# Optimization experiments

Measured on AMD Instinct MI355X. Metric: run time of the kernel, lower is better.

The kernel has to match this reference:

```python
import jax, jax.numpy as jnp
import numpy as np

B, S, H, I, E, K = 4, 2048, 2048, 5632, 8, 2


def setup_inputs() -> dict:
    key = jax.random.key(0)
    k0, k1, k2, k3, k4 = jax.random.split(key, 5)
    std_p = 1.0 / np.sqrt(H)
    return {
        "hidden_states": jax.random.normal(k0, (B, S, H), dtype=jnp.float32),
        "router_w": jax.random.normal(k1, (E, H), dtype=jnp.float32) * 0.02,
        "w_gate": jax.random.normal(k2, (E, H, I), dtype=jnp.float32) * std_p,
        "w_up": jax.random.normal(k3, (E, H, I), dtype=jnp.float32) * std_p,
        "w_down": jax.random.normal(k4, (E, I, H), dtype=jnp.float32) * (1.0 / np.sqrt(I)),
    }


def reference(hidden_states, router_w, w_gate, w_up, w_down):
    b, s, h = hidden_states.shape
    x = hidden_states.reshape(-1, h)                       # [T, H]
    router_logits = x @ router_w.T                          # [T, E]
    routing_weights = jax.nn.softmax(router_logits, axis=-1)
    top_w, top_i = jax.lax.top_k(routing_weights, K)        # [T, K]
    top_w = top_w / jnp.sum(top_w, axis=-1, keepdims=True)  # renormalize over top-k
    # combine[t, e] = sum_k top_w[t, k] * (top_i[t, k] == e)
    combine = jnp.sum(jax.nn.one_hot(top_i, E, dtype=top_w.dtype) * top_w[..., None], axis=1)  # [T, E]
    out = jnp.zeros_like(x)
    for e in range(E):  # small fixed expert count
        # SwiGLU expert MLP: down(silu(gate(x)) * up(x))
        act = jax.nn.silu(x @ w_gate[e]) * (x @ w_up[e])    # [T, I]
        out = out + (act @ w_down[e]) * combine[:, e:e + 1]
    return (out.reshape(b, s, h),
            router_logits.reshape(b, s, E),
            top_i.reshape(b, s, K),
            top_w.reshape(b, s, K))
```

## Files before the change

### kernel.cpp

```cpp
#include <hip/hip_runtime.h>
#include <hip/hip_bf16.h>
#include <stdint.h>

#define NTOK 8192
#define HD   2048
#define ID   5632
#define NE   8
#define NASSIGN (NTOK * 2)
#define MAXT256 (NASSIGN / 256 + NE)

typedef __attribute__((ext_vector_type(8))) short  bf16x8;
typedef __attribute__((ext_vector_type(4))) float  f32x4;
typedef __attribute__((ext_vector_type(8))) unsigned short u16x8;

__device__ __forceinline__ unsigned short f2bf(float f) {
  union { float f; unsigned int u; } c; c.f = f;
  unsigned int lsb = (c.u >> 16) & 1u;
  return (unsigned short)((c.u + 0x7fffu + lsb) >> 16);
}
__device__ __forceinline__ float bf2f(unsigned short u) {
  union { float f; unsigned int u; } c; c.u = ((unsigned int)u) << 16;
  return c.f;
}

__device__ __forceinline__ void async16(const void* g, void* l) {
  __builtin_amdgcn_global_load_lds(
      (const __attribute__((address_space(1))) void*)g,
      (__attribute__((address_space(3))) void*)l, 16, 0, 0);
}

__global__ __launch_bounds__(256) void k_router(
    const float* __restrict__ x, const float* __restrict__ rw,
    float* __restrict__ out_logits, float* __restrict__ out_topi,
    float* __restrict__ out_topw,
    int* __restrict__ tk_e, float* __restrict__ tk_w, int* __restrict__ cnts)
{
  const int wid = threadIdx.x >> 6, lane = threadIdx.x & 63;
  const int t = blockIdx.x * 4 + wid;
  const float* xr = x + (size_t)t * HD;
  float acc[NE];
#pragma unroll
  for (int e = 0; e < NE; e++) acc[e] = 0.f;
#pragma unroll
  for (int i = 0; i < 8; i++) {
    const int col = lane * 4 + i * 256;
    const float4 xv = *(const float4*)(xr + col);
#pragma unroll
    for (int e = 0; e < NE; e++) {
      const float4 wv = *(const float4*)(rw + e * HD + col);
      acc[e] += xv.x * wv.x + xv.y * wv.y + xv.z * wv.z + xv.w * wv.w;
    }
  }
#pragma unroll
  for (int e = 0; e < NE; e++)
    for (int o = 32; o >= 1; o >>= 1) acc[e] += __shfl_xor(acc[e], o, 64);

  if (lane == 0) {
    int i1 = 0;
#pragma unroll
    for (int e = 1; e < NE; e++) if (acc[e] > acc[i1]) i1 = e;
    int i2 = (i1 == 0) ? 1 : 0;
#pragma unroll
    for (int e = 0; e < NE; e++) if (e != i1 && acc[e] > acc[i2]) i2 = e;
    float p2 = __expf(acc[i2] - acc[i1]);
    float s  = 1.f + p2;
    float w1 = 1.f / s, w2 = p2 / s;
#pragma unroll
    for (int e = 0; e < NE; e++) out_logits[(size_t)t * NE + e] = acc[e];
    out_topi[t * 2 + 0] = (float)i1; out_topi[t * 2 + 1] = (float)i2;
    out_topw[t * 2 + 0] = w1;        out_topw[t * 2 + 1] = w2;
    tk_e[t * 2 + 0] = i1; tk_e[t * 2 + 1] = i2;
    tk_w[t * 2 + 0] = w1; tk_w[t * 2 + 1] = w2;
    atomicAdd(&cnts[i1], 1); atomicAdd(&cnts[i2], 1);
  }
}

__global__ void k_scan(const int* __restrict__ cnts, int* __restrict__ offs,
                       int* __restrict__ cursor, int* __restrict__ tile_e,
                       int* __restrict__ tile_rt, int* __restrict__ ntiles) {
  if (threadIdx.x == 0) {
    int s = 0, nt = 0;
    for (int e = 0; e < NE; e++) {
      offs[e] = s; cursor[e] = s;
      int ntl = (cnts[e] + 255) >> 8;
      for (int i = 0; i < ntl; i++) { tile_e[nt] = e; tile_rt[nt] = i; nt++; }
      s += cnts[e];
    }
    ntiles[0] = nt;
  }
}

__global__ void k_assign(const int* __restrict__ tk_e, const float* __restrict__ tk_w,
                         int* __restrict__ cursor, int* __restrict__ perm,
                         float* __restrict__ pw, int* __restrict__ inv) {
  int t = blockIdx.x * 256 + threadIdx.x;
  if (t >= NTOK) return;
#pragma unroll
  for (int k = 0; k < 2; k++) {
    int e = tk_e[t * 2 + k];
    int pos = atomicAdd(&cursor[e], 1);
    perm[pos] = t;
    pw[pos] = tk_w[t * 2 + k];
    inv[t * 2 + k] = pos;
  }
}

__global__ __launch_bounds__(256) void k_gather(const float* __restrict__ x,
    const int* __restrict__ perm, unsigned short* __restrict__ xg) {
  const int r = blockIdx.x;
  const int tok = perm[r];
  const float* src = x + (size_t)tok * HD;
  unsigned short* dst = xg + (size_t)r * HD;
  const int c = threadIdx.x * 8;
  float4 a = *(const float4*)(src + c);
  float4 b = *(const float4*)(src + c + 4);
  u16x8 o;
  o[0] = f2bf(a.x); o[1] = f2bf(a.y); o[2] = f2bf(a.z); o[3] = f2bf(a.w);
  o[4] = f2bf(b.x); o[5] = f2bf(b.y); o[6] = f2bf(b.z); o[7] = f2bf(b.w);
  *(u16x8*)(dst + c) = o;
}

__global__ __launch_bounds__(256) void k_conv_gu(const float* __restrict__ wg,
    const float* __restrict__ wu, unsigned short* __restrict__ wgT,
    unsigned short* __restrict__ wuT) {
  __shared__ float tl[32][33];
  const int z = blockIdx.z, e = z >> 1;
  const float* in = ((z & 1) ? wu : wg) + (size_t)e * HD * ID;
  unsigned short* out = ((z & 1) ? wuT : wgT) + (size_t)e * (size_t)ID * HD;
  const int tx = threadIdx.x & 31, ty = threadIdx.x >> 5;
  const int c0 = blockIdx.x * 32, r0 = blockIdx.y * 32;
#pragma unroll
  for (int j = 0; j < 4; j++)
    tl[ty + j * 8][tx] = in[(size_t)(r0 + ty + j * 8) * ID + (c0 + tx)];
  __syncthreads();
#pragma unroll
  for (int j = 0; j < 4; j++) {
    int oc = ty + j * 8;
    out[(size_t)(c0 + oc) * HD + (r0 + tx)] = f2bf(tl[tx][oc]);
  }
}

__global__ __launch_bounds__(256) void k_conv_d(const float* __restrict__ wd,
    unsigned short* __restrict__ wdT) {
  __shared__ float tl[32][33];
  const int e = blockIdx.z;
  const float* in = wd + (size_t)e * ID * HD;
  unsigned short* out = wdT + (size_t)e * (size_t)HD * ID;
  const int tx = threadIdx.x & 31, ty = threadIdx.x >> 5;
  const int c0 = blockIdx.x * 32, r0 = blockIdx.y * 32;
#pragma unroll
  for (int j = 0; j < 4; j++)
    tl[ty + j * 8][tx] = in[(size_t)(r0 + ty + j * 8) * HD + (c0 + tx)];
  __syncthreads();
#pragma unroll
  for (int j = 0; j < 4; j++) {
    int oc = ty + j * 8;
    out[(size_t)(c0 + oc) * ID + (r0 + tx)] = f2bf(tl[tx][oc]);
  }
}

#define HB(b,kh,op) (((((b)*2+(kh))*2)+(op))*16384)

template <int EPI, int NMAT, int KMAT>
__global__ __launch_bounds__(512, 2) void k_gemm256(
    const unsigned short* __restrict__ A, const unsigned short* __restrict__ Wbase,
    const int* __restrict__ cnts, const int* __restrict__ offs,
    const int* __restrict__ tile_e, const int* __restrict__ tile_rt,
    const int* __restrict__ ntiles,
    unsigned short* __restrict__ gtmp, unsigned short* __restrict__ gact,
    const float* __restrict__ pw, float* __restrict__ dbuf)
{
  const int ti = blockIdx.y;
  if (ti >= ntiles[0]) return;
  const int e = tile_e[ti], rt = tile_rt[ti];
  const int cnt = cnts[e], off = offs[e];
  const int ct = blockIdx.x;
  const int tid = threadIdx.x;

  __shared__ __align__(16) char smem[131072];

  const unsigned short* W = Wbase + (size_t)e * (size_t)NMAT * KMAT;
  const size_t arow0 = (size_t)off + (size_t)rt * 256;
  const size_t bcol0 = (size_t)ct * 256;

  const int u0 = tid, u1 = 512 + tid;
  const int r0s = ((u0 >> 3) << 1) | (((u0 >> 2) & 1) ^ ((u0 >> 4) & 1));
  const int c0s = ((u0 & 3) ^ (r0s & 3)) * 8;
  const int r1s = ((u1 >> 3) << 1) | (((u1 >> 2) & 1) ^ ((u1 >> 4) & 1));
  const int c1s = ((u1 & 3) ^ (r1s & 3)) * 8;

  const int NT = KMAT / 64, NIT = NT / 2;

  auto STAGE_A = [&](int bb, int kh, int kt) {
    const int kc = kt * 64 + kh * 32;
    async16(A + (arow0 + r0s) * (size_t)KMAT + kc + c0s, smem + HB(bb,kh,0) + tid * 16);
    async16(A + (arow0 + r1s) * (size_t)KMAT + kc + c1s, smem + HB(bb,kh,0) + 8192 + tid * 16);
  };
  auto STAGE_B = [&](int bb, int kh, int kt) {
    const int kc = kt * 64 + kh * 32;
    async16(W + (bcol0 + r0s) * (size_t)KMAT + kc + c0s, smem + HB(bb,kh,1) + tid * 16);
    async16(W + (bcol0 + r1s) * (size_t)KMAT + kc + c1s, smem + HB(bb,kh,1) + 8192 + tid * 16);
  };

  f32x4 acc[8][4];
#pragma unroll
  for (int m = 0; m < 8; m++)
#pragma unroll
    for (int n = 0; n < 4; n++) acc[m][n] = (f32x4)0.f;

  const int lane = tid & 63, wid = tid >> 6;
  const int wm = wid >> 2, wn = wid & 3;
  const int fr = lane & 15;
  const int slotp = (lane >> 4) ^ (fr & 3);
  const int laddr = ((fr << 6) | (slotp << 4)) ^ ((fr & 4) << 4);

  STAGE_A(0,0,0); STAGE_B(0,0,0); STAGE_A(0,1,0); STAGE_B(0,1,0);
  STAGE_A(1,0,1); STAGE_B(1,0,1);
  asm volatile("s_waitcnt vmcnt(4)");
  asm volatile("s_barrier" ::: "memory");

  constexpr int SB[8]  = {1,1,0,0,0,0,1,1};
  constexpr int SOP[8] = {0,1,0,1,0,1,0,1};
  constexpr int SKH[8] = {1,1,0,0,1,1,0,0};
  constexpr int SKO[8] = {1,1,2,2,2,2,3,3};

  bf16x8 bfr[4];
  for (int i = 0; i < NIT; ++i) {
#pragma unroll
    for (int p = 0; p < 8; ++p) {
      const int b = p >> 2, kh = (p >> 1) & 1, mh = p & 1;
      bf16x8 afr[4];
#pragma unroll
      for (int t = 0; t < 4; t++)
        afr[t] = *(const bf16x8*)(smem + HB(b,kh,0) + ((wm*128 + mh*64 + t*16) << 6) + laddr);
      if (mh == 0) {
#pragma unroll
        for (int t = 0; t < 4; t++)
          bfr[t] = *(const bf16x8*)(smem + HB(b,kh,1) + ((wn*64 + t*16) << 6) + laddr);
      }
      {
        int kt = 2 * i + SKO[p]; kt = kt < NT - 1 ? kt : NT - 1;
        if (SOP[p] == 0) STAGE_A(SB[p], SKH[p], kt);
        else             STAGE_B(SB[p], SKH[p], kt);
      }
      asm volatile("s_barrier" ::: "memory");
      __builtin_amdgcn_s_setprio(1);
#pragma unroll
      for (int t = 0; t < 4; t++)
#pragma unroll
        for (int n = 0; n < 4; n++)
          acc[mh*4 + t][n] = __builtin_amdgcn_mfma_f32_16x16x32_bf16(afr[t], bfr[n], acc[mh*4 + t][n], 0, 0, 0);
      __builtin_amdgcn_s_setprio(0);
      if (p == 3 || p == 7) asm volatile("s_waitcnt vmcnt(4)");
      asm volatile("s_barrier" ::: "memory");
    }
  }
  asm volatile("s_waitcnt vmcnt(0)");

  const int crow = (lane >> 4) * 4, ccol = lane & 15;
  const int rbase = rt * 256 + wm * 128;
#pragma unroll
  for (int mt = 0; mt < 8; ++mt) {
#pragma unroll
    for (int j = 0; j < 4; ++j) {
      const int rl = rbase + mt * 16 + crow + j;
      if (rl >= cnt) continue;
      const size_t grow = (size_t)off + rl;
      float wgt = 0.f;
      if (EPI == 2) wgt = pw[grow];
#pragma unroll
      for (int nt = 0; nt < 4; ++nt) {
        const int col = (int)bcol0 + wn * 64 + nt * 16 + ccol;
        const float v = acc[mt][nt][j];
        if (EPI == 0) {
          gtmp[grow * (size_t)NMAT + col] = f2bf(v);
        } else if (EPI == 1) {
          const float g = bf2f(gtmp[grow * (size_t)NMAT + col]);
          const float a = g / (1.f + __expf(-g)) * v;
          gact[grow * (size_t)NMAT + col] = f2bf(a);
        } else {
          dbuf[grow * (size_t)NMAT + col] = v * wgt;
        }
      }
    }
  }
}

__global__ __launch_bounds__(256) void k_combine(const float* __restrict__ dbuf,
    const int* __restrict__ inv, float* __restrict__ out) {
  const int t = blockIdx.x;
  const int p0 = inv[t * 2], p1 = inv[t * 2 + 1];
  const float4* r0 = (const float4*)(dbuf + (size_t)p0 * HD);
  const float4* r1 = (const float4*)(dbuf + (size_t)p1 * HD);
  float4* o = (float4*)(out + (size_t)t * HD);
#pragma unroll
  for (int i = 0; i < 2; i++) {
    int c = threadIdx.x + i * 256;
    float4 a = r0[c], b = r1[c];
    o[c] = make_float4(a.x + b.x, a.y + b.y, a.z + b.z, a.w + b.w);
  }
}

extern "C" void kernel_launch(void* const* d_in, const int* in_sizes, int n_in,
                              void* d_out, int out_size, void* d_ws, size_t ws_size,
                              hipStream_t stream) {
  const float* x  = (const float*)d_in[0];
  const float* rw = (const float*)d_in[1];
  const float* wg = (const float*)d_in[2];
  const float* wu = (const float*)d_in[3];
  const float* wd = (const float*)d_in[4];

  float* outp       = (float*)d_out;
  float* out_logits = outp + (size_t)NTOK * HD;
  float* out_topi   = out_logits + (size_t)NTOK * NE;
  float* out_topw   = out_topi + (size_t)NTOK * 2;

  char* w = (char*)d_ws;
  int*   cnts    = (int*)(w + 0);
  int*   offs    = (int*)(w + 64);
  int*   cursor  = (int*)(w + 128);
  int*   ntiles  = (int*)(w + 192);
  int*   tile_e  = (int*)(w + 256);
  int*   tile_rt = (int*)(w + 1280);
  int*   tk_e    = (int*)(w + 4096);
  float* tk_w    = (float*)(w + 4096 + 65536);
  int*   perm    = (int*)(w + 4096 + 2 * 65536);
  float* pw      = (float*)(w + 4096 + 3 * 65536);
  int*   inv     = (int*)(w + 4096 + 4 * 65536);

  char* big = w + (1 << 20);
  unsigned short* xg = (unsigned short*)big;
  const size_t XG_E = (size_t)(NASSIGN + 256) * HD;
  unsigned short* wgT = xg + XG_E;
  const size_t WT_E = (size_t)NE * ID * HD;
  unsigned short* wuT  = wgT + WT_E;
  unsigned short* wdT  = wuT + WT_E;
  unsigned short* gtmp = wdT + WT_E;
  const size_t GA_E = (size_t)(NASSIGN + 256) * ID;
  unsigned short* gact = gtmp + GA_E;
  float* dbuf = (float*)(gact + GA_E);

  hipMemsetAsync(d_ws, 0, 256, stream);

  k_conv_gu<<<dim3(ID / 32, HD / 32, 2 * NE), 256, 0, stream>>>(wg, wu, wgT, wuT);
  k_conv_d<<<dim3(HD / 32, ID / 32, NE), 256, 0, stream>>>(wd, wdT);

  k_router<<<NTOK / 4, 256, 0, stream>>>(x, rw, out_logits, out_topi, out_topw,
                                         tk_e, tk_w, cnts);
  k_scan<<<1, 64, 0, stream>>>(cnts, offs, cursor, tile_e, tile_rt, ntiles);
  k_assign<<<NTOK / 256, 256, 0, stream>>>(tk_e, tk_w, cursor, perm, pw, inv);
  k_gather<<<NASSIGN, 256, 0, stream>>>(x, perm, xg);

  k_gemm256<0, ID, HD><<<dim3(ID / 256, MAXT256), 512, 0, stream>>>(
      xg, wgT, cnts, offs, tile_e, tile_rt, ntiles, gtmp, nullptr, nullptr, nullptr);
  k_gemm256<1, ID, HD><<<dim3(ID / 256, MAXT256), 512, 0, stream>>>(
      xg, wuT, cnts, offs, tile_e, tile_rt, ntiles, gtmp, gact, nullptr, nullptr);
  k_gemm256<2, HD, ID><<<dim3(HD / 256, MAXT256), 512, 0, stream>>>(
      gact, wdT, cnts, offs, tile_e, tile_rt, ntiles, nullptr, nullptr, pw, dbuf);

  k_combine<<<NTOK, 256, 0, stream>>>(dbuf, inv, outp);
}
```

Before: 2.030 ms.

## Fuse gate and up GEMMs into one kernel sharing A tiles

Merges the separate gate and up projection GEMMs into a single kernel. Each A tile is loaded once and multiplied against both the gate and up weights, with two accumulator sets and the SiLU*up epilogue applied in registers. This removes the bf16 gate intermediate write and read, and halves A-tile traffic for those GEMMs. The grid is also reordered so row tiles vary fastest. The cost is double the accumulator registers and occupancy limited to one block per CU, plus a new three-buffer pipeline with 32-wide k steps.

```diff
diff --git a/kernel.cpp b/kernel.cpp
--- a/kernel.cpp
+++ b/kernel.cpp
@@ -17,10 +17,6 @@
   union { float f; unsigned int u; } c; c.f = f;
   unsigned int lsb = (c.u >> 16) & 1u;
   return (unsigned short)((c.u + 0x7fffu + lsb) >> 16);
-}
-__device__ __forceinline__ float bf2f(unsigned short u) {
-  union { float f; unsigned int u; } c; c.u = ((unsigned int)u) << 16;
-  return c.f;
 }
 
 __device__ __forceinline__ void async16(const void* g, void* l) {
@@ -159,27 +155,24 @@
   }
 }
 
-#define HB(b,kh,op) (((((b)*2+(kh))*2)+(op))*16384)
-
-template <int EPI, int NMAT, int KMAT>
-__global__ __launch_bounds__(512, 2) void k_gemm256(
-    const unsigned short* __restrict__ A, const unsigned short* __restrict__ Wbase,
+__global__ __launch_bounds__(512, 1) void k_gemm_gu256(
+    const unsigned short* __restrict__ A,
+    const unsigned short* __restrict__ BgT, const unsigned short* __restrict__ BuT,
     const int* __restrict__ cnts, const int* __restrict__ offs,
     const int* __restrict__ tile_e, const int* __restrict__ tile_rt,
-    const int* __restrict__ ntiles,
-    unsigned short* __restrict__ gtmp, unsigned short* __restrict__ gact,
-    const float* __restrict__ pw, float* __restrict__ dbuf)
+    const int* __restrict__ ntiles, unsigned short* __restrict__ gact)
 {
-  const int ti = blockIdx.y;
+  const int ti = blockIdx.x;
   if (ti >= ntiles[0]) return;
   const int e = tile_e[ti], rt = tile_rt[ti];
   const int cnt = cnts[e], off = offs[e];
-  const int ct = blockIdx.x;
+  const int ct = blockIdx.y;
   const int tid = threadIdx.x;
 
-  __shared__ __align__(16) char smem[131072];
-
-  const unsigned short* W = Wbase + (size_t)e * (size_t)NMAT * KMAT;
+  __shared__ __align__(16) char smem[9 * 16384];
+
+  const unsigned short* Bg = BgT + (size_t)e * (size_t)ID * HD;
+  const unsigned short* Bu = BuT + (size_t)e * (size_t)ID * HD;
   const size_t arow0 = (size_t)off + (size_t)rt * 256;
   const size_t bcol0 = (size_t)ct * 256;
 
@@ -189,17 +182,136 @@
   const int r1s = ((u1 >> 3) << 1) | (((u1 >> 2) & 1) ^ ((u1 >> 4) & 1));
   const int c1s = ((u1 & 3) ^ (r1s & 3)) * 8;
 
-  const int NT = KMAT / 64, NIT = NT / 2;
+  auto ST = [&](const unsigned short* P, size_t row0, int kc, int chunk) {
+    async16(P + (row0 + r0s) * (size_t)HD + kc + c0s, smem + (chunk << 14) + tid * 16);
+    async16(P + (row0 + r1s) * (size_t)HD + kc + c1s, smem + (chunk << 14) + 8192 + tid * 16);
+  };
+
+  f32x4 accg[8][4], accu[8][4];
+#pragma unroll
+  for (int m = 0; m < 8; m++)
+#pragma unroll
+    for (int n = 0; n < 4; n++) { accg[m][n] = (f32x4)0.f; accu[m][n] = (f32x4)0.f; }
+
+  const int lane = tid & 63, wid = tid >> 6;
+  const int wm = wid >> 2, wn = wid & 3;
+  const int fr = lane & 15;
+  const int slotp = (lane >> 4) ^ (fr & 3);
+  const int laddr = ((fr << 6) | (slotp << 4)) ^ ((fr & 4) << 4);
+
+  const int NT = HD / 32;
+
+  ST(A, arow0, 0, 0);  ST(Bg, bcol0, 0, 1);  ST(Bu, bcol0, 0, 2);
+  ST(A, arow0, 32, 3); ST(Bg, bcol0, 32, 4); ST(Bu, bcol0, 32, 5);
+  asm volatile("s_waitcnt vmcnt(6)");
+  asm volatile("s_barrier" ::: "memory");
+
+#define MFMA16(ACC, MB, FRG) \
+  __builtin_amdgcn_s_setprio(1); \
+  _Pragma("unroll") \
+  for (int t = 0; t < 4; t++) \
+    _Pragma("unroll") \
+    for (int n = 0; n < 4; n++) \
+      ACC[(MB) + t][n] = __builtin_amdgcn_mfma_f32_16x16x32_bf16(afr[t], FRG[n], ACC[(MB) + t][n], 0, 0, 0); \
+  __builtin_amdgcn_s_setprio(0);
+
+  int cb = 0, sb = 2;
+  bf16x8 afr[4], bgr[4], bur[4];
+  for (int i = 0; i < NT; ++i) {
+    const int cb3 = cb * 3, sb3 = sb * 3;
+    int kn = i + 2; kn = kn < NT - 1 ? kn : NT - 1;
+    const int kc2 = kn * 32;
+#pragma unroll
+    for (int t = 0; t < 4; t++)
+      afr[t] = *(const bf16x8*)(smem + ((cb3 + 0) << 14) + ((wm * 128 + t * 16) << 6) + laddr);
+#pragma unroll
+    for (int t = 0; t < 4; t++)
+      bgr[t] = *(const bf16x8*)(smem + ((cb3 + 1) << 14) + ((wn * 64 + t * 16) << 6) + laddr);
+    ST(A, arow0, kc2, sb3 + 0);
+    asm volatile("s_barrier" ::: "memory");
+    MFMA16(accg, 0, bgr)
+    asm volatile("s_barrier" ::: "memory");
+#pragma unroll
+    for (int t = 0; t < 4; t++)
+      bur[t] = *(const bf16x8*)(smem + ((cb3 + 2) << 14) + ((wn * 64 + t * 16) << 6) + laddr);
+    ST(Bg, bcol0, kc2, sb3 + 1);
+    asm volatile("s_barrier" ::: "memory");
+    MFMA16(accu, 0, bur)
+    asm volatile("s_barrier" ::: "memory");
+#pragma unroll
+    for (int t = 0; t < 4; t++)
+      afr[t] = *(const bf16x8*)(smem + ((cb3 + 0) << 14) + ((wm * 128 + 64 + t * 16) << 6) + laddr);
+    ST(Bu, bcol0, kc2, sb3 + 2);
+    asm volatile("s_barrier" ::: "memory");
+    MFMA16(accg, 4, bgr)
+    asm volatile("s_barrier" ::: "memory");
+    asm volatile("s_waitcnt vmcnt(6)");
+    MFMA16(accu, 4, bur)
+    asm volatile("s_barrier" ::: "memory");
+    sb = cb; cb = cb + 1 == 3 ? 0 : cb + 1;
+  }
+  asm volatile("s_waitcnt vmcnt(0)");
+
+  const int crow = (lane >> 4) * 4, ccol = lane & 15;
+  const int rbase = rt * 256 + wm * 128;
+#pragma unroll
+  for (int mt = 0; mt < 8; ++mt) {
+#pragma unroll
+    for (int j = 0; j < 4; ++j) {
+      const int rl = rbase + mt * 16 + crow + j;
+      if (rl >= cnt) continue;
+      const size_t grow = (size_t)off + rl;
+#pragma unroll
+      for (int nt = 0; nt < 4; ++nt) {
+        const int col = (int)bcol0 + wn * 64 + nt * 16 + ccol;
+        const float g = accg[mt][nt][j], u = accu[mt][nt][j];
+        const float a = g / (1.f + __expf(-g)) * u;
+        gact[grow * (size_t)ID + col] = f2bf(a);
+      }
+    }
+  }
+#undef MFMA16
+}
+
+#define HB(b,kh,op) (((((b)*2+(kh))*2)+(op))*16384)
+__global__ __launch_bounds__(512, 2) void k_gemm_dn256(
+    const unsigned short* __restrict__ A,
+    const unsigned short* __restrict__ Wbase,
+    const int* __restrict__ cnts, const int* __restrict__ offs,
+    const int* __restrict__ tile_e, const int* __restrict__ tile_rt,
+    const int* __restrict__ ntiles,
+    const float* __restrict__ pw, float* __restrict__ dbuf)
+{
+  const int ti = blockIdx.x;
+  if (ti >= ntiles[0]) return;
+  const int e = tile_e[ti], rt = tile_rt[ti];
+  const int cnt = cnts[e], off = offs[e];
+  const int ct = blockIdx.y;
+  const int tid = threadIdx.x;
+
+  __shared__ __align__(16) char smem[131072];
+
+  const unsigned short* W = Wbase + (size_t)e * (size_t)HD * ID;
+  const size_t arow0 = (size_t)off + (size_t)rt * 256;
+  const size_t bcol0 = (size_t)ct * 256;
+
+  const int u0 = tid, u1 = 512 + tid;
+  const int r0s = ((u0 >> 3) << 1) | (((u0 >> 2) & 1) ^ ((u0 >> 4) & 1));
+  const int c0s = ((u0 & 3) ^ (r0s & 3)) * 8;
+  const int r1s = ((u1 >> 3) << 1) | (((u1 >> 2) & 1) ^ ((u1 >> 4) & 1));
+  const int c1s = ((u1 & 3) ^ (r1s & 3)) * 8;
+
+  const int NT = ID / 64, NIT = NT / 2;
 
   auto STAGE_A = [&](int bb, int kh, int kt) {
     const int kc = kt * 64 + kh * 32;
-    async16(A + (arow0 + r0s) * (size_t)KMAT + kc + c0s, smem + HB(bb,kh,0) + tid * 16);
-    async16(A + (arow0 + r1s) * (size_t)KMAT + kc + c1s, smem + HB(bb,kh,0) + 8192 + tid * 16);
+    async16(A + (arow0 + r0s) * (size_t)ID + kc + c0s, smem + HB(bb,kh,0) + tid * 16);
+    async16(A + (arow0 + r1s) * (size_t)ID + kc + c1s, smem + HB(bb,kh,0) + 8192 + tid * 16);
   };
   auto STAGE_B = [&](int bb, int kh, int kt) {
     const int kc = kt * 64 + kh * 32;
-    async16(W + (bcol0 + r0s) * (size_t)KMAT + kc + c0s, smem + HB(bb,kh,1) + tid * 16);
-    async16(W + (bcol0 + r1s) * (size_t)KMAT + kc + c1s, smem + HB(bb,kh,1) + 8192 + tid * 16);
+    async16(W + (bcol0 + r0s) * (size_t)ID + kc + c0s, smem + HB(bb,kh,1) + tid * 16);
+    async16(W + (bcol0 + r1s) * (size_t)ID + kc + c1s, smem + HB(bb,kh,1) + 8192 + tid * 16);
   };
 
   f32x4 acc[8][4];
@@ -266,21 +378,11 @@
       const int rl = rbase + mt * 16 + crow + j;
       if (rl >= cnt) continue;
       const size_t grow = (size_t)off + rl;
-      float wgt = 0.f;
-      if (EPI == 2) wgt = pw[grow];
+      const float wgt = pw[grow];
 #pragma unroll
       for (int nt = 0; nt < 4; ++nt) {
         const int col = (int)bcol0 + wn * 64 + nt * 16 + ccol;
-        const float v = acc[mt][nt][j];
-        if (EPI == 0) {
-          gtmp[grow * (size_t)NMAT + col] = f2bf(v);
-        } else if (EPI == 1) {
-          const float g = bf2f(gtmp[grow * (size_t)NMAT + col]);
-          const float a = g / (1.f + __expf(-g)) * v;
-          gact[grow * (size_t)NMAT + col] = f2bf(a);
-        } else {
-          dbuf[grow * (size_t)NMAT + col] = v * wgt;
-        }
+        dbuf[grow * (size_t)HD + col] = acc[mt][nt][j] * wgt;
       }
     }
   }
@@ -335,9 +437,8 @@
   const size_t WT_E = (size_t)NE * ID * HD;
   unsigned short* wuT  = wgT + WT_E;
   unsigned short* wdT  = wuT + WT_E;
-  unsigned short* gtmp = wdT + WT_E;
+  unsigned short* gact = wdT + WT_E;
   const size_t GA_E = (size_t)(NASSIGN + 256) * ID;
-  unsigned short* gact = gtmp + GA_E;
   float* dbuf = (float*)(gact + GA_E);
 
   hipMemsetAsync(d_ws, 0, 256, stream);
@@ -351,12 +452,10 @@
   k_assign<<<NTOK / 256, 256, 0, stream>>>(tk_e, tk_w, cursor, perm, pw, inv);
   k_gather<<<NASSIGN, 256, 0, stream>>>(x, perm, xg);
 
-  k_gemm256<0, ID, HD><<<dim3(ID / 256, MAXT256), 512, 0, stream>>>(
-      xg, wgT, cnts, offs, tile_e, tile_rt, ntiles, gtmp, nullptr, nullptr, nullptr);
-  k_gemm256<1, ID, HD><<<dim3(ID / 256, MAXT256), 512, 0, stream>>>(
-      xg, wuT, cnts, offs, tile_e, tile_rt, ntiles, gtmp, gact, nullptr, nullptr);
-  k_gemm256<2, HD, ID><<<dim3(HD / 256, MAXT256), 512, 0, stream>>>(
-      gact, wdT, cnts, offs, tile_e, tile_rt, ntiles, nullptr, nullptr, pw, dbuf);
+  k_gemm_gu256<<<dim3(MAXT256, ID / 256), 512, 0, stream>>>(
+      xg, wgT, wuT, cnts, offs, tile_e, tile_rt, ntiles, gact);
+  k_gemm_dn256<<<dim3(MAXT256, HD / 256), 512, 0, stream>>>(
+      gact, wdT, cnts, offs, tile_e, tile_rt, ntiles, pw, dbuf);
 
   k_combine<<<NTOK, 256, 0, stream>>>(dbuf, inv, outp);
 }
```

Result: slower. 6.558 ms (+223.1%).
